# Kernel tuning notes

Measured on AMD Instinct MI355X. Metric: run time of the kernel, lower is better.

The kernel has to match this reference:

```python
import jax, jax.numpy as jnp
import numpy as np

N = 100000      # num_nodes
E = 1600000     # num edges (avg degree 16)
R = 400         # num_relations passed to GCNLayer (masks at R and 2R)
DIN, DH, DOUT = 128, 128, 128
EPS = 1e-5


def setup_inputs() -> dict:
    key = jax.random.key(0)
    ks = jax.random.split(key, 8)
    src = jax.random.randint(ks[0], (E,), 0, N)
    dst = jax.random.randint(ks[1], (E,), 0, N)
    rel = jax.random.randint(ks[2], (E,), 0, 2 * R + 1)  # covers orig/inverse/self-loop buckets
    edges = jnp.stack([src, rel, dst], axis=1)  # [E,3] = (head, rel, tail)

    def xinit(k, shape, fan_in):
        return jax.random.normal(k, shape, jnp.float32) * (1.0 / np.sqrt(fan_in))

    node_emb = xinit(ks[3], (N, DIN), DIN)
    # stacked relation-branch linears: [3, out, in] = (original, inverse, self_loop)
    W1 = xinit(ks[4], (3, DH, DIN), DIN)
    b1 = jnp.zeros((3, DH), jnp.float32)
    Ws1 = xinit(ks[5], (DH, DIN), DIN)
    bs1 = jnp.zeros((DH,), jnp.float32)
    g1 = jnp.ones((DH,), jnp.float32)
    be1 = jnp.zeros((DH,), jnp.float32)
    W2 = xinit(ks[6], (3, DOUT, DH), DH)
    b2 = jnp.zeros((3, DOUT), jnp.float32)
    Ws2 = xinit(ks[7], (DOUT, DH), DH)
    bs2 = jnp.zeros((DOUT,), jnp.float32)
    g2 = jnp.ones((DOUT,), jnp.float32)
    be2 = jnp.zeros((DOUT,), jnp.float32)
    return dict(edges=edges, node_emb=node_emb, W1=W1, b1=b1, Ws1=Ws1, bs1=bs1,
                g1=g1, be1=be1, W2=W2, b2=b2, Ws2=Ws2, bs2=bs2, g2=g2, be2=be2)


def _gcn_layer(x, src, dst, bucket, W, b):
    # Project node features once per relation branch (same math as projecting
    # gathered src features, but N << E so this is cheaper): Y[r] = x @ W[r].T + b[r]
    Y = jnp.einsum('nd,rod->rno', x, W) + b[:, None, :]     # [3, N, out]
    msgs = Y[bucket, src]                                   # [E, out] gather by (branch, src)
    n = x.shape[0]
    out = jax.ops.segment_sum(msgs, dst, num_segments=n)    # scatter-add to dst
    cnt = jax.ops.segment_sum(jnp.ones_like(dst, dtype=x.dtype), dst, num_segments=n)
    out = out / jnp.maximum(cnt, 1.0)[:, None]              # degree norm, clamp min=1
    return jax.nn.relu(out)


def _layer_norm(x, g, b):
    m = jnp.mean(x, axis=-1, keepdims=True)
    v = jnp.mean((x - m) ** 2, axis=-1, keepdims=True)
    return (x - m) * jax.lax.rsqrt(v + EPS) * g + b


def reference(edges, node_emb, W1, b1, Ws1, bs1, g1, be1, W2, b2, Ws2, bs2, g2, be2):
    src, rel, dst = edges[:, 0], edges[:, 1], edges[:, 2]
    # bucket: 0=original (rel<R), 1=inverse (R<=rel<2R), 2=self-loop (rel>=2R)
    bucket = (rel >= R).astype(jnp.int32) + (rel >= 2 * R).astype(jnp.int32)

    x1 = _gcn_layer(node_emb, src, dst, bucket, W1, b1)
    x1 = x1 + node_emb @ Ws1.T + bs1                # skip1
    x1 = _layer_norm(x1, g1, be1)                   # dropout: eval-mode identity

    x2 = _gcn_layer(x1, src, dst, bucket, W2, b2)
    x2 = x2 + x1 @ Ws2.T + bs2                      # skip2
    x2 = _layer_norm(x2, g2, be2)
    return x2
```

## Files before the change

### kernel.cpp

```cpp
#include <hip/hip_runtime.h>
#include <stdint.h>

typedef unsigned int uint;
typedef unsigned short ushort;

#define NNODES 100000
#define NPAD   100096
#define NEDGES 1600000
#define RCONST 400
#define CAP    64
#define ZROW   NNODES

#define NBKT   196
#define NBLK_A 512
#define EPB    3125
#define RUNCAP 64

typedef __attribute__((ext_vector_type(8))) short short8;
typedef __attribute__((ext_vector_type(4))) float f32x4;
typedef __attribute__((ext_vector_type(2))) float f32x2;

__device__ __forceinline__ float bflo(uint u){ union{uint i;float f;}c; c.i=u<<16; return c.f; }
__device__ __forceinline__ float bfhi(uint u){ union{uint i;float f;}c; c.i=u&0xFFFF0000u; return c.f; }
__device__ __forceinline__ ushort f2bf(float f){ union{uint i;float ff;}c; c.ff=f; uint u=c.i;
    return (ushort)((u + 0x7FFFu + ((u>>16)&1u))>>16); }
__device__ __forceinline__ uint pack2(float lo, float hi){
    return (uint)f2bf(lo) | ((uint)f2bf(hi)<<16); }


__global__ __launch_bounds__(256) void binfill_kernel(const int* __restrict__ edges,
                                                      int* __restrict__ runcnt,
                                                      uint* __restrict__ binned) {
    __shared__ int pos[NBKT];
    int blk = blockIdx.x, tid = threadIdx.x;
    for (int i = tid; i < NBKT; i += 256) pos[i] = 0;
    __syncthreads();
    int start = blk * EPB;
    for (int i = tid; i < EPB; i += 256) {
        int e = start + i;
        int src = edges[e * 3];
        int rel = edges[e * 3 + 1];
        int dst = edges[e * 3 + 2];
        int bkt = (rel >= RCONST) + (rel >= 2 * RCONST);
        int b = dst >> 9, off = dst & 511;
        int p = atomicAdd(&pos[b], 1);
        if (p < RUNCAP)
            binned[((size_t)b * NBLK_A + blk) * RUNCAP + p] =
                (uint)src | ((uint)bkt << 17) | ((uint)off << 19);
    }
    __syncthreads();
    for (int i = tid; i < NBKT; i += 256)
        runcnt[blk * NBKT + i] = min(pos[i], RUNCAP);
}


__global__ __launch_bounds__(256) void scatter_kernel(const uint* __restrict__ binned,
                                                      const int* __restrict__ runcnt,
                                                      int* __restrict__ elist,
                                                      uint* __restrict__ segp,
                                                      float4* __restrict__ cnts) {
    __shared__ int cnt3[512][4];
    __shared__ int cur[512][4];
    int b = blockIdx.x, tid = threadIdx.x;
    int base = b << 9;
    for (int i = tid; i < 512; i += 256) { cnt3[i][0] = 0; cnt3[i][1] = 0; cnt3[i][2] = 0; }
    __syncthreads();
    #pragma unroll
    for (int rr = 0; rr < 2; ++rr) {
        int r = tid * 2 + rr;
        int n = runcnt[r * NBKT + b];
        const uint* p = binned + ((size_t)b * NBLK_A + r) * RUNCAP;
        for (int i = 0; i < n; ++i) {
            uint e = p[i];
            atomicAdd(&cnt3[e >> 19][(e >> 17) & 3], 1);
        }
    }
    __syncthreads();
    for (int i = tid; i < 512; i += 256) {
        int node = base + i;
        if (node >= NPAD) continue;
        int c0 = cnt3[i][0], c1 = cnt3[i][1], c2 = cnt3[i][2];
        int n0 = min((c0 + 1) & ~1, 64);
        int n1 = min((c1 + 1) & ~1, 64 - n0);
        int n2 = min((c2 + 1) & ~1, 64 - n0 - n1);
        int s1 = n0, s2 = n0 + n1, tot = n0 + n1 + n2;
        cur[i][0] = 0; cur[i][1] = s1; cur[i][2] = s2;
        int* er = elist + (size_t)node * 64;
        for (int j = min(c0, n0); j < n0; ++j) er[j] = ZROW;
        for (int j = min(c1, n1); j < n1; ++j) er[s1 + j] = ZROW;
        for (int j = min(c2, n2); j < n2; ++j) er[s2 + j] = ZROW;
        cnt3[i][0] = s1; cnt3[i][1] = s2; cnt3[i][2] = tot;
        segp[node] = (uint)n0 | ((uint)n1 << 8) | ((uint)n2 << 16);
        float4 v;
        v.x = (float)c0; v.y = (float)c1; v.z = (float)c2;
        v.w = 1.0f / fmaxf((float)(c0 + c1 + c2), 1.0f);
        cnts[node] = v;
    }
    __syncthreads();
    #pragma unroll
    for (int rr = 0; rr < 2; ++rr) {
        int r = tid * 2 + rr;
        int n = runcnt[r * NBKT + b];
        const uint* p = binned + ((size_t)b * NBLK_A + r) * RUNCAP;
        for (int i = 0; i < n; ++i) {
            uint e = p[i];
            int off = (int)(e >> 19), bk = (int)((e >> 17) & 3);
            int pos = atomicAdd(&cur[off][bk], 1);
            if (pos < cnt3[off][bk])
                elist[(size_t)(base + off) * 64 + pos] = (int)(e & 0x1FFFFu);
        }
    }
}


__global__ __launch_bounds__(256) void convx_kernel(const float* __restrict__ x,
                                                    uint* __restrict__ xb) {
    size_t i = (size_t)blockIdx.x * 256 + threadIdx.x;
    if (i < (size_t)NPAD * 64) {
        uint val = 0;
        if (i < (size_t)NNODES * 64) {
            float2 f = *(const float2*)&x[i * 2];
            val = pack2(f.x, f.y);
        }
        xb[i] = val;
    }
}

__global__ __launch_bounds__(256) void wconv_kernel(const float* __restrict__ W,
                                                    const float* __restrict__ Ws,
                                                    uint* __restrict__ Wb) {
    int i = blockIdx.x * 256 + threadIdx.x;
    if (i < 128 * 256) {
        int n = i >> 8, kp = i & 255, k = kp * 2;
        float v0, v1;
        if (k < 384) {
            int r = k >> 7, kk = k & 127;
            const float* p = W + r * 16384 + n * 128 + kk;
            v0 = p[0]; v1 = p[1];
        } else {
            const float* p = Ws + n * 128 + (k - 384);
            v0 = p[0]; v1 = p[1];
        }
        Wb[i] = pack2(v0, v1);
    }
}


__global__ __launch_bounds__(256) void gather_kernel(
    const uint* __restrict__ xb,
    const uint* __restrict__ segp,
    const int*  __restrict__ elist,
    const float4* __restrict__ cnts,
    uint* __restrict__ Ab) {
    int tid = threadIdx.x;
    int w = tid >> 6, lane = tid & 63;
    int node = blockIdx.x * 4 + w;
    uint sp = __builtin_amdgcn_readfirstlane(segp[node]);
    float inv = cnts[node].w;
    int ve = elist[(size_t)node * 64 + lane];
    int half = lane >> 5, hl = lane & 31;
    const char* xrow = (const char*)xb + (hl << 3);

    f32x2 a00 = {0.f, 0.f}, a01 = {0.f, 0.f};
    f32x2 a10 = {0.f, 0.f}, a11 = {0.f, 0.f};
    f32x2 a20 = {0.f, 0.f}, a21 = {0.f, 0.f};
    int n0 = (int)(sp & 255), n1 = (int)((sp >> 8) & 255), n2 = (int)((sp >> 16) & 255);
    int eb = 0;

    #define SEG(NB, A0, A1)                                                   \
    for (int j = 0; j < NB; j += 2) {                                         \
        int sA = __builtin_amdgcn_readlane(ve, eb + j);                       \
        int sB = __builtin_amdgcn_readlane(ve, eb + j + 1);                   \
        int ss = half ? sB : sA;                                              \
        uint2 u = *(const uint2*)(xrow + ((size_t)((uint)ss << 8)));          \
        f32x2 f0 = {bflo(u.x), bfhi(u.x)};                                    \
        f32x2 f1 = {bflo(u.y), bfhi(u.y)};                                    \
        A0 += f0; A1 += f1;                                                   \
    }                                                                         \
    eb += NB;

    SEG(n0, a00, a01)
    SEG(n1, a10, a11)
    SEG(n2, a20, a21)
    #undef SEG

    #define COMB(A) { f32x2 t; t.x = __shfl_xor(A.x, 32); t.y = __shfl_xor(A.y, 32); \
                      A += t; A *= inv; }
    COMB(a00) COMB(a01) COMB(a10) COMB(a11) COMB(a20) COMB(a21)
    #undef COMB

    if (half == 0) {
        size_t ab = (size_t)node * 192 + hl * 2;
        uint2 v0 = { pack2(a00.x, a00.y), pack2(a01.x, a01.y) };
        *(uint2*)&Ab[ab] = v0;
        uint2 v1 = { pack2(a10.x, a10.y), pack2(a11.x, a11.y) };
        *(uint2*)&Ab[ab + 64] = v1;
        uint2 v2 = { pack2(a20.x, a20.y), pack2(a21.x, a21.y) };
        *(uint2*)&Ab[ab + 128] = v2;
    }
}


template<bool OUT_BF16>
__global__ __launch_bounds__(256, 3) void gemm_kernel(
    const ushort* __restrict__ Ab,
    const ushort* __restrict__ xb,
    const ushort* __restrict__ Wb,
    const float* __restrict__ bia,
    const float* __restrict__ bs,
    const float* __restrict__ g,
    const float* __restrict__ be,
    const float4* __restrict__ cnts,
    void* __restrict__ out) {
    __shared__ ushort lA[64 * 64];
    __shared__ ushort lB[128 * 64];
    __shared__ float sS1[4][64], sS2[4][64];
    __shared__ float sMean[64], sRstd[64];

    int tid = threadIdx.x;
    int w = tid >> 6, lane = tid & 63;
    int wn = w;
    int quad = lane >> 4, l15 = lane & 15;
    int node0 = blockIdx.x * 64;

    int arow = tid >> 2, aseg = tid & 3;
    int brow = tid >> 1, bseg = (tid & 1) * 4;
    uint swzA = (uint)((arow & 7) << 4);
    uint swzB = (uint)((brow & 7) << 4);
    uint swzR = (uint)((l15 & 7) << 4);

    const ushort* gA = Ab + (size_t)node0 * 384;
    const ushort* gX = xb + (size_t)node0 * 128;

    f32x4 accm[4][2], accq[4][2];
    f32x4 zero = {0.f, 0.f, 0.f, 0.f};
    #pragma unroll
    for (int i = 0; i < 4; ++i)
        #pragma unroll
        for (int j = 0; j < 2; ++j) { accm[i][j] = zero; accq[i][j] = zero; }

    uint4 ra0, ra1, rb0, rb1, rb2, rb3;
    auto load_chunk = [&](int t) {
        const ushort* srcA; size_t strA;
        if (t < 6) { srcA = gA + t * 64;       strA = 384; }
        else       { srcA = gX + (t - 6) * 64; strA = 128; }
        const ushort* pa = srcA + (size_t)arow * strA + aseg * 8;
        ra0 = *(const uint4*)(pa);
        ra1 = *(const uint4*)(pa + 32);
        const ushort* pb = Wb + t * 64 + (size_t)brow * 512 + bseg * 8;
        rb0 = *(const uint4*)(pb);
        rb1 = *(const uint4*)(pb + 8);
        rb2 = *(const uint4*)(pb + 16);
        rb3 = *(const uint4*)(pb + 24);
    };
    auto compute = [&](f32x4 (&acc)[4][2]) {
        #pragma unroll
        for (int ks = 0; ks < 2; ++ks) {
            short8 aF[4], bF[2];
            #pragma unroll
            for (int mt = 0; mt < 4; ++mt) {
                int row = mt * 16 + l15;
                aF[mt] = *(const short8*)((const char*)lA + row * 128 +
                                          (((uint)(ks * 64 + quad * 16)) ^ swzR));
            }
            #pragma unroll
            for (int nt = 0; nt < 2; ++nt) {
                int row = wn * 32 + nt * 16 + l15;
                bF[nt] = *(const short8*)((const char*)lB + row * 128 +
                                          (((uint)(ks * 64 + quad * 16)) ^ swzR));
            }
            #pragma unroll
            for (int mt = 0; mt < 4; ++mt)
                #pragma unroll
                for (int nt = 0; nt < 2; ++nt)
                    acc[mt][nt] = __builtin_amdgcn_mfma_f32_16x16x32_bf16(
                        aF[mt], bF[nt], acc[mt][nt], 0, 0, 0);
        }
    };

    load_chunk(0);
    for (int t = 0; t < 8; ++t) {
        if (t) __syncthreads();
        {
            char* bA = (char*)lA + arow * 128;
            *(uint4*)(bA + (((uint)(aseg * 16)) ^ swzA))       = ra0;
            *(uint4*)(bA + (((uint)((aseg + 4) * 16)) ^ swzA)) = ra1;
            char* bB = (char*)lB + brow * 128;
            *(uint4*)(bB + (((uint)((bseg + 0) * 16)) ^ swzB)) = rb0;
            *(uint4*)(bB + (((uint)((bseg + 1) * 16)) ^ swzB)) = rb1;
            *(uint4*)(bB + (((uint)((bseg + 2) * 16)) ^ swzB)) = rb2;
            *(uint4*)(bB + (((uint)((bseg + 3) * 16)) ^ swzB)) = rb3;
        }
        __syncthreads();
        if (t < 7) load_chunk(t + 1);
        if (t < 6) compute(accm); else compute(accq);
    }

    int nl0 = wn * 32 + l15;
    float pb0[2], pb1[2], pb2[2], pbs[2], pg[2], pbe[2];
    #pragma unroll
    for (int nt = 0; nt < 2; ++nt) {
        int nl = nl0 + nt * 16;
        pb0[nt] = bia[nl]; pb1[nt] = bia[128 + nl]; pb2[nt] = bia[256 + nl];
        pbs[nt] = bs[nl];  pg[nt] = g[nl];          pbe[nt] = be[nl];
    }
    #pragma unroll
    for (int mt = 0; mt < 4; ++mt) {
        #pragma unroll
        for (int r = 0; r < 4; ++r) {
            int ml = mt * 16 + quad * 4 + r;
            float4 c4 = cnts[node0 + ml];
            float s1 = 0.f, s2 = 0.f;
            #pragma unroll
            for (int nt = 0; nt < 2; ++nt) {
                float bd = (c4.x * pb0[nt] + c4.y * pb1[nt] + c4.z * pb2[nt]) * c4.w;
                float v = fmaxf(accm[mt][nt][r] + bd, 0.f) + accq[mt][nt][r] + pbs[nt];
                accm[mt][nt][r] = v;
                s1 += v; s2 += v * v;
            }
            #pragma unroll
            for (int mask = 1; mask < 16; mask <<= 1) {
                s1 += __shfl_xor(s1, mask);
                s2 += __shfl_xor(s2, mask);
            }
            if (l15 == 0) { sS1[wn][ml] = s1; sS2[wn][ml] = s2; }
        }
    }
    __syncthreads();
    if (tid < 64) {
        float s1 = sS1[0][tid] + sS1[1][tid] + sS1[2][tid] + sS1[3][tid];
        float s2 = sS2[0][tid] + sS2[1][tid] + sS2[2][tid] + sS2[3][tid];
        float mean = s1 * (1.f / 128.f);
        float var = s2 * (1.f / 128.f) - mean * mean;
        sMean[tid] = mean;
        sRstd[tid] = rsqrtf(var + 1e-5f);
    }
    __syncthreads();
    #pragma unroll
    for (int mt = 0; mt < 4; ++mt) {
        #pragma unroll
        for (int r = 0; r < 4; ++r) {
            int ml = mt * 16 + quad * 4 + r;
            int node = node0 + ml;
            float mn = sMean[ml], rs = sRstd[ml];
            #pragma unroll
            for (int nt = 0; nt < 2; ++nt) {
                float v = (accm[mt][nt][r] - mn) * rs * pg[nt] + pbe[nt];
                if (OUT_BF16) {
                    float vh = __shfl_xor(v, 1);
                    if (!(l15 & 1)) {
                        uint val = (node < NNODES) ? pack2(v, vh) : 0u;
                        uint* o = (uint*)out;
                        o[(size_t)node * 64 + wn * 16 + nt * 8 + (l15 >> 1)] = val;
                    }
                } else {
                    if (node < NNODES) {
                        float* o = (float*)out;
                        o[(size_t)node * 128 + nl0 + nt * 16] = v;
                    }
                }
            }
        }
    }
}


extern "C" void kernel_launch(void* const* d_in, const int* in_sizes, int n_in,
                              void* d_out, int out_size, void* d_ws, size_t ws_size,
                              hipStream_t stream) {
    (void)in_sizes; (void)n_in; (void)out_size; (void)ws_size;

    const int*   edges = (const int*)d_in[0];
    const float* xemb  = (const float*)d_in[1];
    const float* W1  = (const float*)d_in[2];
    const float* b1  = (const float*)d_in[3];
    const float* Ws1 = (const float*)d_in[4];
    const float* bs1 = (const float*)d_in[5];
    const float* g1  = (const float*)d_in[6];
    const float* be1 = (const float*)d_in[7];
    const float* W2  = (const float*)d_in[8];
    const float* b2  = (const float*)d_in[9];
    const float* Ws2 = (const float*)d_in[10];
    const float* bs2 = (const float*)d_in[11];
    const float* g2  = (const float*)d_in[12];
    const float* be2 = (const float*)d_in[13];

    char* ws = (char*)d_ws;
    auto take = [&](size_t bytes) {
        char* p = ws;
        ws += (bytes + 255) & ~(size_t)255;
        return p;
    };
    int*    elist  = (int*)take((size_t)NPAD * CAP * 4);
    uint*   segp   = (uint*)take((size_t)NPAD * 4);
    float4* cnts   = (float4*)take((size_t)NPAD * 16);
    uint*   xb0    = (uint*)take((size_t)NPAD * 128 * 2);
    uint*   xb1    = (uint*)take((size_t)NPAD * 128 * 2);
    uint*   Ab     = (uint*)take((size_t)NPAD * 384 * 2);
    uint*   Wb1    = (uint*)take((size_t)128 * 512 * 2);
    uint*   Wb2    = (uint*)take((size_t)128 * 512 * 2);
    int*    runcnt = (int*)take((size_t)NBLK_A * NBKT * 4);
    uint*   binned = (uint*)take((size_t)NBKT * NBLK_A * RUNCAP * 4);

    binfill_kernel<<<NBLK_A, 256, 0, stream>>>(edges, runcnt, binned);
    scatter_kernel<<<NBKT, 256, 0, stream>>>(binned, runcnt, elist, segp, cnts);

    convx_kernel<<<(NPAD * 64) / 256, 256, 0, stream>>>(xemb, xb0);
    wconv_kernel<<<128, 256, 0, stream>>>(W1, Ws1, Wb1);
    wconv_kernel<<<128, 256, 0, stream>>>(W2, Ws2, Wb2);

    gather_kernel<<<NNODES / 4, 256, 0, stream>>>(xb0, segp, elist, cnts, Ab);
    gemm_kernel<true><<<NPAD / 64, 256, 0, stream>>>(
        (const ushort*)Ab, (const ushort*)xb0, (const ushort*)Wb1,
        b1, bs1, g1, be1, cnts, xb1);

    gather_kernel<<<NNODES / 4, 256, 0, stream>>>(xb1, segp, elist, cnts, Ab);
    gemm_kernel<false><<<NPAD / 64, 256, 0, stream>>>(
        (const ushort*)Ab, (const ushort*)xb1, (const ushort*)Wb2,
        b2, bs2, g2, be2, cnts, d_out);
}
```

Baseline: 421.6 us.

## Fuse neighbor gather into GEMM kernel and encode bucket in edge list

The separate gather and GEMM kernels become one fused kernel per layer. Each wave aggregates the neighbor features of 8 nodes straight into LDS as bf16 A tiles, and the kernel then runs the MFMA GEMM, the skip connection and the layernorm. This removes the global round trip of the large Ab intermediate. The edge list now keeps the bucket bits next to the source index, so aggregation uses branchless per-bucket masks over a single loop instead of three segment loops. In exchange, LDS use per block grows to hold 64x384 A tiles and blocks have 512 threads, which limits occupancy for the latency-bound gather.

```diff
diff --git a/kernel.cpp b/kernel.cpp
--- a/kernel.cpp
+++ b/kernel.cpp
@@ -18,7 +18,6 @@
 
 typedef __attribute__((ext_vector_type(8))) short short8;
 typedef __attribute__((ext_vector_type(4))) float f32x4;
-typedef __attribute__((ext_vector_type(2))) float f32x2;
 
 __device__ __forceinline__ float bflo(uint u){ union{uint i;float f;}c; c.i=u<<16; return c.f; }
 __device__ __forceinline__ float bfhi(uint u){ union{uint i;float f;}c; c.i=u&0xFFFF0000u; return c.f; }
@@ -83,13 +82,13 @@
         int n0 = min((c0 + 1) & ~1, 64);
         int n1 = min((c1 + 1) & ~1, 64 - n0);
         int n2 = min((c2 + 1) & ~1, 64 - n0 - n1);
-        int s1 = n0, s2 = n0 + n1, tot = n0 + n1 + n2;
+        int s1 = n0, s2 = n0 + n1;
         cur[i][0] = 0; cur[i][1] = s1; cur[i][2] = s2;
         int* er = elist + (size_t)node * 64;
         for (int j = min(c0, n0); j < n0; ++j) er[j] = ZROW;
         for (int j = min(c1, n1); j < n1; ++j) er[s1 + j] = ZROW;
         for (int j = min(c2, n2); j < n2; ++j) er[s2 + j] = ZROW;
-        cnt3[i][0] = s1; cnt3[i][1] = s2; cnt3[i][2] = tot;
+        cnt3[i][0] = s1; cnt3[i][1] = s2; cnt3[i][2] = s2 + n2;
         segp[node] = (uint)n0 | ((uint)n1 << 8) | ((uint)n2 << 16);
         float4 v;
         v.x = (float)c0; v.y = (float)c1; v.z = (float)c2;
@@ -107,7 +106,7 @@
             int off = (int)(e >> 19), bk = (int)((e >> 17) & 3);
             int pos = atomicAdd(&cur[off][bk], 1);
             if (pos < cnt3[off][bk])
-                elist[(size_t)(base + off) * 64 + pos] = (int)(e & 0x1FFFFu);
+                elist[(size_t)(base + off) * 64 + pos] = (int)(e & 0x7FFFFu);
         }
     }
 }
@@ -146,122 +145,139 @@
 }
 
 
-__global__ __launch_bounds__(256) void gather_kernel(
-    const uint* __restrict__ xb,
+template<bool OUT_BF16>
+__global__ __launch_bounds__(512, 2) void fused_kernel(
+    const uint* __restrict__ xbu,
+    const ushort* __restrict__ Wb,
     const uint* __restrict__ segp,
     const int*  __restrict__ elist,
     const float4* __restrict__ cnts,
-    uint* __restrict__ Ab) {
-    int tid = threadIdx.x;
-    int w = tid >> 6, lane = tid & 63;
-    int node = blockIdx.x * 4 + w;
-    uint sp = __builtin_amdgcn_readfirstlane(segp[node]);
-    float inv = cnts[node].w;
-    int ve = elist[(size_t)node * 64 + lane];
-    int half = lane >> 5, hl = lane & 31;
-    const char* xrow = (const char*)xb + (hl << 3);
-
-    f32x2 a00 = {0.f, 0.f}, a01 = {0.f, 0.f};
-    f32x2 a10 = {0.f, 0.f}, a11 = {0.f, 0.f};
-    f32x2 a20 = {0.f, 0.f}, a21 = {0.f, 0.f};
-    int n0 = (int)(sp & 255), n1 = (int)((sp >> 8) & 255), n2 = (int)((sp >> 16) & 255);
-    int eb = 0;
-
-    #define SEG(NB, A0, A1)                                                   \
-    for (int j = 0; j < NB; j += 2) {                                         \
-        int sA = __builtin_amdgcn_readlane(ve, eb + j);                       \
-        int sB = __builtin_amdgcn_readlane(ve, eb + j + 1);                   \
-        int ss = half ? sB : sA;                                              \
-        uint2 u = *(const uint2*)(xrow + ((size_t)((uint)ss << 8)));          \
-        f32x2 f0 = {bflo(u.x), bfhi(u.x)};                                    \
-        f32x2 f1 = {bflo(u.y), bfhi(u.y)};                                    \
-        A0 += f0; A1 += f1;                                                   \
-    }                                                                         \
-    eb += NB;
-
-    SEG(n0, a00, a01)
-    SEG(n1, a10, a11)
-    SEG(n2, a20, a21)
-    #undef SEG
-
-    #define COMB(A) { f32x2 t; t.x = __shfl_xor(A.x, 32); t.y = __shfl_xor(A.y, 32); \
-                      A += t; A *= inv; }
-    COMB(a00) COMB(a01) COMB(a10) COMB(a11) COMB(a20) COMB(a21)
-    #undef COMB
-
-    if (half == 0) {
-        size_t ab = (size_t)node * 192 + hl * 2;
-        uint2 v0 = { pack2(a00.x, a00.y), pack2(a01.x, a01.y) };
-        *(uint2*)&Ab[ab] = v0;
-        uint2 v1 = { pack2(a10.x, a10.y), pack2(a11.x, a11.y) };
-        *(uint2*)&Ab[ab + 64] = v1;
-        uint2 v2 = { pack2(a20.x, a20.y), pack2(a21.x, a21.y) };
-        *(uint2*)&Ab[ab + 128] = v2;
-    }
-}
-
-
-template<bool OUT_BF16>
-__global__ __launch_bounds__(256, 3) void gemm_kernel(
-    const ushort* __restrict__ Ab,
-    const ushort* __restrict__ xb,
-    const ushort* __restrict__ Wb,
     const float* __restrict__ bia,
     const float* __restrict__ bs,
     const float* __restrict__ g,
     const float* __restrict__ be,
-    const float4* __restrict__ cnts,
     void* __restrict__ out) {
-    __shared__ ushort lA[64 * 64];
+    __shared__ ushort lA[64 * 384];
     __shared__ ushort lB[128 * 64];
     __shared__ float sS1[4][64], sS2[4][64];
     __shared__ float sMean[64], sRstd[64];
 
+    const ushort* xbs = (const ushort*)xbu;
     int tid = threadIdx.x;
     int w = tid >> 6, lane = tid & 63;
-    int wn = w;
+    int wm = w >> 2, wn = w & 3;
     int quad = lane >> 4, l15 = lane & 15;
     int node0 = blockIdx.x * 64;
-
-    int arow = tid >> 2, aseg = tid & 3;
-    int brow = tid >> 1, bseg = (tid & 1) * 4;
-    uint swzA = (uint)((arow & 7) << 4);
+    uint swzR = (uint)((l15 & 7) << 4);
+
+    int brow = tid >> 2, bseg2 = (tid & 3) * 2;
     uint swzB = (uint)((brow & 7) << 4);
-    uint swzR = (uint)((l15 & 7) << 4);
-
-    const ushort* gA = Ab + (size_t)node0 * 384;
-    const ushort* gX = xb + (size_t)node0 * 128;
-
-    f32x4 accm[4][2], accq[4][2];
+    uint4 rb0, rb1;
+    auto loadB = [&](int t) {
+        const ushort* pb = Wb + t * 64 + (size_t)brow * 512 + bseg2 * 8;
+        rb0 = *(const uint4*)(pb);
+        rb1 = *(const uint4*)(pb + 8);
+    };
+    auto storeB = [&]() {
+        char* bB = (char*)lB + brow * 128;
+        *(uint4*)(bB + (((uint)(bseg2 * 16)) ^ swzB))       = rb0;
+        *(uint4*)(bB + (((uint)((bseg2 + 1) * 16)) ^ swzB)) = rb1;
+    };
+
+    loadB(0);
+
+    for (int i = 0; i < 8; ++i) {
+        int arow = w * 8 + i;
+        int node = node0 + arow;
+        uint sp = segp[node];
+        int tot = (int)(sp & 255) + (int)((sp >> 8) & 255) + (int)((sp >> 16) & 255);
+        float inv = cnts[node].w;
+        int ve = elist[(size_t)node * 64 + lane];
+
+        float a0l = 0.f, a0h = 0.f, a1l = 0.f, a1h = 0.f, a2l = 0.f, a2h = 0.f;
+        int j = 0;
+        for (; j + 4 <= tot; j += 4) {
+            int e0 = __builtin_amdgcn_readlane(ve, j);
+            int e1 = __builtin_amdgcn_readlane(ve, j + 1);
+            int e2 = __builtin_amdgcn_readlane(ve, j + 2);
+            int e3 = __builtin_amdgcn_readlane(ve, j + 3);
+            int s0 = e0 & 0x1FFFF, k0 = e0 >> 17;
+            int s1 = e1 & 0x1FFFF, k1 = e1 >> 17;
+            int s2 = e2 & 0x1FFFF, k2 = e2 >> 17;
+            int s3 = e3 & 0x1FFFF, k3 = e3 >> 17;
+            uint u0 = xbu[((size_t)s0 << 6) + lane];
+            uint u1 = xbu[((size_t)s1 << 6) + lane];
+            uint u2 = xbu[((size_t)s2 << 6) + lane];
+            uint u3 = xbu[((size_t)s3 << 6) + lane];
+
+            float q00 = (k0 == 0) ? 1.f : 0.f, q01 = (k0 == 1) ? 1.f : 0.f, q02 = (k0 == 2) ? 1.f : 0.f;
+            float q10 = (k1 == 0) ? 1.f : 0.f, q11 = (k1 == 1) ? 1.f : 0.f, q12 = (k1 == 2) ? 1.f : 0.f;
+            float q20 = (k2 == 0) ? 1.f : 0.f, q21 = (k2 == 1) ? 1.f : 0.f, q22 = (k2 == 2) ? 1.f : 0.f;
+            float q30 = (k3 == 0) ? 1.f : 0.f, q31 = (k3 == 1) ? 1.f : 0.f, q32 = (k3 == 2) ? 1.f : 0.f;
+
+            float f0l = bflo(u0), f0h = bfhi(u0);
+            float f1l = bflo(u1), f1h = bfhi(u1);
+            float f2l = bflo(u2), f2h = bfhi(u2);
+            float f3l = bflo(u3), f3h = bfhi(u3);
+
+            a0l = fmaf(q00, f0l, a0l); a1l = fmaf(q01, f0l, a1l); a2l = fmaf(q02, f0l, a2l);
+            a0h = fmaf(q00, f0h, a0h); a1h = fmaf(q01, f0h, a1h); a2h = fmaf(q02, f0h, a2h);
+            a0l = fmaf(q10, f1l, a0l); a1l = fmaf(q11, f1l, a1l); a2l = fmaf(q12, f1l, a2l);
+            a0h = fmaf(q10, f1h, a0h); a1h = fmaf(q11, f1h, a1h); a2h = fmaf(q12, f1h, a2h);
+            a0l = fmaf(q20, f2l, a0l); a1l = fmaf(q21, f2l, a1l); a2l = fmaf(q22, f2l, a2l);
+            a0h = fmaf(q20, f2h, a0h); a1h = fmaf(q21, f2h, a1h); a2h = fmaf(q22, f2h, a2h);
+            a0l = fmaf(q30, f3l, a0l); a1l = fmaf(q31, f3l, a1l); a2l = fmaf(q32, f3l, a2l);
+            a0h = fmaf(q30, f3h, a0h); a1h = fmaf(q31, f3h, a1h); a2h = fmaf(q32, f3h, a2h);
+        }
+        if (j < tot) {
+            int e0 = __builtin_amdgcn_readlane(ve, j);
+            int e1 = __builtin_amdgcn_readlane(ve, j + 1);
+            int s0 = e0 & 0x1FFFF, k0 = e0 >> 17;
+            int s1 = e1 & 0x1FFFF, k1 = e1 >> 17;
+            uint u0 = xbu[((size_t)s0 << 6) + lane];
+            uint u1 = xbu[((size_t)s1 << 6) + lane];
+            float q00 = (k0 == 0) ? 1.f : 0.f, q01 = (k0 == 1) ? 1.f : 0.f, q02 = (k0 == 2) ? 1.f : 0.f;
+            float q10 = (k1 == 0) ? 1.f : 0.f, q11 = (k1 == 1) ? 1.f : 0.f, q12 = (k1 == 2) ? 1.f : 0.f;
+            float f0l = bflo(u0), f0h = bfhi(u0);
+            float f1l = bflo(u1), f1h = bfhi(u1);
+            a0l = fmaf(q00, f0l, a0l); a1l = fmaf(q01, f0l, a1l); a2l = fmaf(q02, f0l, a2l);
+            a0h = fmaf(q00, f0h, a0h); a1h = fmaf(q01, f0h, a1h); a2h = fmaf(q02, f0h, a2h);
+            a0l = fmaf(q10, f1l, a0l); a1l = fmaf(q11, f1l, a1l); a2l = fmaf(q12, f1l, a2l);
+            a0h = fmaf(q10, f1h, a0h); a1h = fmaf(q11, f1h, a1h); a2h = fmaf(q12, f1h, a2h);
+        }
+        uint sw = (uint)((arow & 7) << 4);
+        char* rA = (char*)lA + arow * 768;
+        *(uint*)(rA + (((uint)(lane * 4)) ^ sw))       = pack2(a0l * inv, a0h * inv);
+        *(uint*)(rA + (((uint)(256 + lane * 4)) ^ sw)) = pack2(a1l * inv, a1h * inv);
+        *(uint*)(rA + (((uint)(512 + lane * 4)) ^ sw)) = pack2(a2l * inv, a2h * inv);
+    }
+
+    f32x4 accm[2][2], accq[2][2];
     f32x4 zero = {0.f, 0.f, 0.f, 0.f};
     #pragma unroll
-    for (int i = 0; i < 4; ++i)
+    for (int i = 0; i < 2; ++i)
         #pragma unroll
         for (int j = 0; j < 2; ++j) { accm[i][j] = zero; accq[i][j] = zero; }
 
-    uint4 ra0, ra1, rb0, rb1, rb2, rb3;
-    auto load_chunk = [&](int t) {
-        const ushort* srcA; size_t strA;
-        if (t < 6) { srcA = gA + t * 64;       strA = 384; }
-        else       { srcA = gX + (t - 6) * 64; strA = 128; }
-        const ushort* pa = srcA + (size_t)arow * strA + aseg * 8;
-        ra0 = *(const uint4*)(pa);
-        ra1 = *(const uint4*)(pa + 32);
-        const ushort* pb = Wb + t * 64 + (size_t)brow * 512 + bseg * 8;
-        rb0 = *(const uint4*)(pb);
-        rb1 = *(const uint4*)(pb + 8);
-        rb2 = *(const uint4*)(pb + 16);
-        rb3 = *(const uint4*)(pb + 24);
-    };
-    auto compute = [&](f32x4 (&acc)[4][2]) {
+    __syncthreads();
+    storeB();
+    __syncthreads();
+
+    #pragma unroll
+    for (int kc = 0; kc < 8; ++kc) {
+        if (kc < 7) loadB(kc + 1);
         #pragma unroll
         for (int ks = 0; ks < 2; ++ks) {
-            short8 aF[4], bF[2];
-            #pragma unroll
-            for (int mt = 0; mt < 4; ++mt) {
-                int row = mt * 16 + l15;
-                aF[mt] = *(const short8*)((const char*)lA + row * 128 +
-                                          (((uint)(ks * 64 + quad * 16)) ^ swzR));
+            short8 aF[2], bF[2];
+            #pragma unroll
+            for (int mt = 0; mt < 2; ++mt) {
+                int row = wm * 32 + mt * 16 + l15;
+                if (kc < 6)
+                    aF[mt] = *(const short8*)((const char*)lA + row * 768 +
+                        (((uint)((kc >> 1) * 256 + (kc & 1) * 128 + ks * 64 + quad * 16)) ^ swzR));
+                else
+                    aF[mt] = *(const short8*)(xbs + (size_t)(node0 + row) * 128 +
+                                              (kc - 6) * 64 + ks * 32 + quad * 8);
             }
             #pragma unroll
             for (int nt = 0; nt < 2; ++nt) {
@@ -270,30 +286,18 @@
                                           (((uint)(ks * 64 + quad * 16)) ^ swzR));
             }
             #pragma unroll
-            for (int mt = 0; mt < 4; ++mt)
+            for (int mt = 0; mt < 2; ++mt)
                 #pragma unroll
-                for (int nt = 0; nt < 2; ++nt)
-                    acc[mt][nt] = __builtin_amdgcn_mfma_f32_16x16x32_bf16(
-                        aF[mt], bF[nt], acc[mt][nt], 0, 0, 0);
-        }
-    };
-
-    load_chunk(0);
-    for (int t = 0; t < 8; ++t) {
-        if (t) __syncthreads();
-        {
-            char* bA = (char*)lA + arow * 128;
-            *(uint4*)(bA + (((uint)(aseg * 16)) ^ swzA))       = ra0;
-            *(uint4*)(bA + (((uint)((aseg + 4) * 16)) ^ swzA)) = ra1;
-            char* bB = (char*)lB + brow * 128;
-            *(uint4*)(bB + (((uint)((bseg + 0) * 16)) ^ swzB)) = rb0;
-            *(uint4*)(bB + (((uint)((bseg + 1) * 16)) ^ swzB)) = rb1;
-            *(uint4*)(bB + (((uint)((bseg + 2) * 16)) ^ swzB)) = rb2;
-            *(uint4*)(bB + (((uint)((bseg + 3) * 16)) ^ swzB)) = rb3;
-        }
-        __syncthreads();
-        if (t < 7) load_chunk(t + 1);
-        if (t < 6) compute(accm); else compute(accq);
+                for (int nt = 0; nt < 2; ++nt) {
+                    if (kc < 6)
+                        accm[mt][nt] = __builtin_amdgcn_mfma_f32_16x16x32_bf16(
+                            aF[mt], bF[nt], accm[mt][nt], 0, 0, 0);
+                    else
+                        accq[mt][nt] = __builtin_amdgcn_mfma_f32_16x16x32_bf16(
+                            aF[mt], bF[nt], accq[mt][nt], 0, 0, 0);
+                }
+        }
+        if (kc < 7) { __syncthreads(); storeB(); __syncthreads(); }
     }
 
     int nl0 = wn * 32 + l15;
@@ -305,10 +309,10 @@
         pbs[nt] = bs[nl];  pg[nt] = g[nl];          pbe[nt] = be[nl];
     }
     #pragma unroll
-    for (int mt = 0; mt < 4; ++mt) {
+    for (int mt = 0; mt < 2; ++mt) {
         #pragma unroll
         for (int r = 0; r < 4; ++r) {
-            int ml = mt * 16 + quad * 4 + r;
+            int ml = wm * 32 + mt * 16 + quad * 4 + r;
             float4 c4 = cnts[node0 + ml];
             float s1 = 0.f, s2 = 0.f;
             #pragma unroll
@@ -337,10 +341,10 @@
     }
     __syncthreads();
     #pragma unroll
-    for (int mt = 0; mt < 4; ++mt) {
+    for (int mt = 0; mt < 2; ++mt) {
         #pragma unroll
         for (int r = 0; r < 4; ++r) {
-            int ml = mt * 16 + quad * 4 + r;
+            int ml = wm * 32 + mt * 16 + quad * 4 + r;
             int node = node0 + ml;
             float mn = sMean[ml], rs = sRstd[ml];
             #pragma unroll
@@ -396,7 +400,6 @@
     float4* cnts   = (float4*)take((size_t)NPAD * 16);
     uint*   xb0    = (uint*)take((size_t)NPAD * 128 * 2);
     uint*   xb1    = (uint*)take((size_t)NPAD * 128 * 2);
-    uint*   Ab     = (uint*)take((size_t)NPAD * 384 * 2);
     uint*   Wb1    = (uint*)take((size_t)128 * 512 * 2);
     uint*   Wb2    = (uint*)take((size_t)128 * 512 * 2);
     int*    runcnt = (int*)take((size_t)NBLK_A * NBKT * 4);
@@ -409,13 +412,11 @@
     wconv_kernel<<<128, 256, 0, stream>>>(W1, Ws1, Wb1);
     wconv_kernel<<<128, 256, 0, stream>>>(W2, Ws2, Wb2);
 
-    gather_kernel<<<NNODES / 4, 256, 0, stream>>>(xb0, segp, elist, cnts, Ab);
-    gemm_kernel<true><<<NPAD / 64, 256, 0, stream>>>(
-        (const ushort*)Ab, (const ushort*)xb0, (const ushort*)Wb1,
-        b1, bs1, g1, be1, cnts, xb1);
-
-    gather_kernel<<<NNODES / 4, 256, 0, stream>>>(xb1, segp, elist, cnts, Ab);
-    gemm_kernel<false><<<NPAD / 64, 256, 0, stream>>>(
-        (const ushort*)Ab, (const ushort*)xb1, (const ushort*)Wb2,
-        b2, bs2, g2, be2, cnts, d_out);
-}
+    fused_kernel<true><<<NPAD / 64, 512, 0, stream>>>(
+        xb0, (const ushort*)Wb1, segp, elist, cnts,
+        b1, bs1, g1, be1, xb1);
+
+    fused_kernel<false><<<NPAD / 64, 512, 0, stream>>>(
+        xb1, (const ushort*)Wb2, segp, elist, cnts,
+        b2, bs2, g2, be2, d_out);
+}
```

Result: slower. 448.1 us (+6.3%).
